# Optimization experiments

Hardware: AMD Instinct MI355X
Metric: run time of the kernel (lower is better)

Reference implementation:

```python
import jax, jax.numpy as jnp
import numpy as np

N_SIGMA = 1
K_MAX = 8          # max number of non-zero instance ids
FG_W = 1.0         # foreground_weight
W_INST, W_VAR, W_SEED = 1.0, 10.0, 1.0


def _lovasz_hinge_flat(logits, labels_f):
    # logits, labels_f: [P] flat; standard Lovasz hinge (descending-error sort)
    signs = 2.0 * labels_f - 1.0
    errors = 1.0 - logits * signs
    perm = jnp.argsort(-errors)
    errors_sorted = errors[perm]
    gt_sorted = labels_f[perm]
    gts = gt_sorted.sum()
    cum = jnp.cumsum(gt_sorted)
    intersection = gts - cum
    union = gts + jnp.cumsum(1.0 - gt_sorted)
    jaccard = 1.0 - intersection / union
    grad = jnp.concatenate([jaccard[:1], jaccard[1:] - jaccard[:-1]])
    return jnp.sum(jax.nn.relu(errors_sorted) * jax.lax.stop_gradient(grad))


def _spatial_emb_loss(prediction, instances, labels):
    B, C, H, W = prediction.shape
    inst = instances[:, 0]  # [B,H,W]
    # coordinate buffer: linspace over the full 1024x2048 grid, then sliced
    xm = jnp.linspace(0.0, 2.0, 2048)[:W]
    ym = jnp.linspace(0.0, 1.0, 1024)[:H]
    xym = jnp.stack([jnp.broadcast_to(xm[None, :], (H, W)),
                     jnp.broadcast_to(ym[:, None], (H, W))])  # [2,H,W]
    ids = jnp.arange(1, K_MAX + 1)

    def per_image(pred, ins, lab):
        spatial_emb = jnp.tanh(pred[0:2]) + xym            # [2,H,W]
        sigma = pred[2]                                     # [H,W] (n_sigma=1)
        seed = jax.nn.sigmoid(pred[3])                      # [H,W]
        bg = (lab == 0)
        seed_loss_bg = jnp.sum(jnp.where(bg, seed ** 2, 0.0))
        masks = (ins[None] == ids[:, None, None])           # [K,H,W]
        mf = masks.astype(pred.dtype)
        counts = mf.sum((1, 2))                             # [K]
        present = counts > 0
        cnt = jnp.maximum(counts, 1.0)
        # to_center=True: center = mean of xym over instance pixels
        center = jnp.einsum('chw,khw->kc', xym, mf) / cnt[:, None]   # [K,2]
        s_mean = jnp.einsum('hw,khw->k', sigma, mf) / cnt            # [K]
        var_k = jnp.einsum('khw,khw->k',
                           (sigma[None] - jax.lax.stop_gradient(s_mean)[:, None, None]) ** 2,
                           mf) / cnt
        s_exp = jnp.exp(10.0 * s_mean)                                # [K]
        d2 = jnp.sum((spatial_emb[None] - center[:, :, None, None]) ** 2, axis=1)  # [K,H,W]
        dist = jnp.exp(-s_exp[:, None, None] * d2)                    # [K,H,W]
        lov = jax.vmap(_lovasz_hinge_flat)(2.0 * dist.reshape(K_MAX, -1) - 1.0,
                                           mf.reshape(K_MAX, -1))     # [K]
        seed_fg = jnp.einsum('khw,khw->k',
                             (seed[None] - jax.lax.stop_gradient(dist)) ** 2, mf)
        objf = jnp.maximum(present.sum().astype(pred.dtype), 1.0)
        inst_loss = jnp.where(present, lov, 0.0).sum() / objf
        var_loss = jnp.where(present, var_k, 0.0).sum() / objf
        seed_loss = (seed_loss_bg + FG_W * jnp.where(present, seed_fg, 0.0).sum()) / (H * W)
        return W_INST * inst_loss + W_VAR * var_loss + W_SEED * seed_loss

    per = jax.vmap(per_image)(prediction, inst, labels)
    return per.mean() + 0.0 * prediction.sum()


def setup_inputs() -> dict:
    key = jax.random.key(0)
    k1, k2, k3 = jax.random.split(key, 3)
    B, H, W = 4, 512, 1024
    prediction = jax.random.normal(k1, (B, 2 + N_SIGMA + 1, H, W), dtype=jnp.float32)
    instances = jax.random.randint(k2, (B, 1, H, W), 0, K_MAX + 1, dtype=jnp.int32)
    labels = jax.random.randint(k3, (B, H, W), 0, 2, dtype=jnp.int32)
    return {"prediction": prediction, "instances": instances, "labels": labels}


def reference(prediction, instances, labels):
    return _spatial_emb_loss(prediction, instances, labels)
```

## Files before the change

### kernel.cpp

```cpp
#include <hip/hip_runtime.h>
#include <math.h>

namespace {
constexpr int B_ = 4, K_ = 8, H_ = 512, W_ = 1024;
constexpr int N_ = H_ * W_;
constexpr int M_ = 256;
constexpr int MP_ = M_ + 1;
constexpr int BK_ = B_ * K_;
constexpr int KM_ = K_ * M_;

constexpr int HB_ = 1024;
constexpr int HBPB_ = HB_ / B_;
constexpr int HCH_ = N_ / HBPB_;
constexpr int SB_ = 1024;
constexpr int SBPB_ = SB_ / B_;
constexpr int SCH_ = N_ / SBPB_;
constexpr int NSTAT = 41;

constexpr size_t PART_BYTES = (size_t)HB_ * KM_ * 4;
constexpr size_t SFG_OFF_B  = PART_BYTES;
constexpr size_t PSTAT_OFF_B = SFG_OFF_B + (size_t)BK_ * HBPB_ * 4;
constexpr size_t WSF_OFF_B  = PSTAT_OFF_B + (size_t)B_ * NSTAT * SBPB_ * 4;

constexpr int CNT_OFF  = 0;
constexpr int OBJF_OFF = 32;
}

__device__ __forceinline__ float fsigmoid_(float x) { return 1.0f / (1.0f + __expf(-x)); }
__device__ __forceinline__ float ftanh_(float x) { return 1.0f - 2.0f / (__expf(2.0f * x) + 1.0f); }

__global__ __launch_bounds__(256) void stats_kernel(const float* __restrict__ pred,
                                                    const int* __restrict__ inst,
                                                    const int* __restrict__ lab,
                                                    float* __restrict__ pstat,
                                                    float* __restrict__ out) {
    int tid = threadIdx.x;
    if (blockIdx.x == 0 && tid == 0) out[0] = 0.0f;
    int b = blockIdx.x >> 8;
    int blk = blockIdx.x & (SBPB_ - 1);
    int pix0 = blk * SCH_;

    const float* sigp = pred + ((long long)b * 4 + 2) * N_;
    const float* p3p  = pred + ((long long)b * 4 + 3) * N_;
    const int*   insp = inst + (long long)b * N_;
    const int*   labp = lab  + (long long)b * N_;

    float acc[NSTAT];
#pragma unroll
    for (int i = 0; i < NSTAT; i++) acc[i] = 0.0f;

#pragma unroll
    for (int it = 0; it < SCH_ / (256 * 4); it++) {
        int base = pix0 + (it * 256 + tid) * 4;
        float4 sg = *(const float4*)(sigp + base);
        float4 q3 = *(const float4*)(p3p + base);
        int4 in4 = *(const int4*)(insp + base);
        int4 lb4 = *(const int4*)(labp + base);
        float ss[4] = {sg.x, sg.y, sg.z, sg.w};
        float qq[4] = {q3.x, q3.y, q3.z, q3.w};
        int ii[4] = {in4.x, in4.y, in4.z, in4.w};
        int ll[4] = {lb4.x, lb4.y, lb4.z, lb4.w};
#pragma unroll
        for (int j = 0; j < 4; j++) {
            int pix = base + j;
            float xm = (float)(pix & (W_ - 1)) * (2.0f / 2047.0f);
            float ym = (float)(pix >> 10) * (1.0f / 1023.0f);
            float seed = fsigmoid_(qq[j]);
            if (ll[j] == 0) acc[40] += seed * seed;
            float s = ss[j];
#pragma unroll
            for (int k = 0; k < K_; k++) {
                float m = (ii[j] == k + 1) ? 1.0f : 0.0f;
                acc[k * 5]     += m;
                acc[k * 5 + 1] += m * xm;
                acc[k * 5 + 2] += m * ym;
                acc[k * 5 + 3] += m * s;
                acc[k * 5 + 4] += m * s * s;
            }
        }
    }
#pragma unroll
    for (int i = 0; i < NSTAT; i++) {
        float v = acc[i];
#pragma unroll
        for (int off = 32; off; off >>= 1) v += __shfl_down(v, off, 64);
        acc[i] = v;
    }
    __shared__ float xw[4][NSTAT];
    if ((tid & 63) == 0) {
        int w = tid >> 6;
#pragma unroll
        for (int i = 0; i < NSTAT; i++) xw[w][i] = acc[i];
    }
    __syncthreads();
    if (tid < NSTAT)
        pstat[((b * NSTAT + tid) << 8) + blk] =
            xw[0][tid] + xw[1][tid] + xw[2][tid] + xw[3][tid];
}

__global__ __launch_bounds__(256) void hist_kernel(const float* __restrict__ pred,
                                                   const int* __restrict__ inst,
                                                   const float* __restrict__ pstat,
                                                   float* __restrict__ wsf,
                                                   unsigned int* __restrict__ partial,
                                                   float* __restrict__ sfgpart,
                                                   float* __restrict__ out) {
    __shared__ float sq[NSTAT][4];
    __shared__ float ssum[NSTAT];
    __shared__ float prm[K_][4];
    __shared__ float svar[K_];
    __shared__ int spres[K_];
    __shared__ unsigned int hsh[K_ * MP_];
    __shared__ float xfg[4][K_];

    int tid = threadIdx.x;
    int b = blockIdx.x >> 8;
    int blk = blockIdx.x & (HBPB_ - 1);
    int pix0 = blk * HCH_;

    if (tid < NSTAT * 4) {
        int row = tid >> 2, q = tid & 3;
        const float4* p = (const float4*)(pstat + ((size_t)(b * NSTAT + row) << 8)) + q * 16;
        float4 a = {0, 0, 0, 0};
#pragma unroll
        for (int j = 0; j < 16; j++) {
            float4 v = p[j];
            a.x += v.x; a.y += v.y; a.z += v.z; a.w += v.w;
        }
        sq[row][q] = (a.x + a.y) + (a.z + a.w);
    }
    for (int i = tid; i < K_ * MP_; i += 256) hsh[i] = 0u;
    __syncthreads();
    if (tid < NSTAT) ssum[tid] = (sq[tid][0] + sq[tid][1]) + (sq[tid][2] + sq[tid][3]);
    __syncthreads();
    if (tid < K_) {
        float counts = ssum[tid * 5];
        float cnt = fmaxf(counts, 1.0f);
        float smean = ssum[tid * 5 + 3] / cnt;
        prm[tid][0] = ssum[tid * 5 + 1] / cnt;
        prm[tid][1] = ssum[tid * 5 + 2] / cnt;
        prm[tid][2] = expf(10.0f * smean);
        prm[tid][3] = counts;
        if (blk == 0) {
            svar[tid] = (counts > 0.0f) ? ssum[tid * 5 + 4] / cnt - smean * smean : 0.0f;
            spres[tid] = counts > 0.0f ? 1 : 0;
            wsf[CNT_OFF + b * K_ + tid] = counts;
        }
    }
    __syncthreads();
    if (blk == 0 && tid == 0) {
        float np = 0.0f, vl = 0.0f;
#pragma unroll
        for (int k = 0; k < K_; k++) { np += (float)spres[k]; vl += svar[k]; }
        float objf = fmaxf(np, 1.0f);
        wsf[OBJF_OFF + b] = objf;
        atomicAdd(out, (10.0f * vl / objf + ssum[40] / (float)N_) * (1.0f / (float)B_));
    }

    float cx[K_], cy[K_], sxp[K_];
    bool prs[K_];
#pragma unroll
    for (int k = 0; k < K_; k++) {
        cx[k] = prm[k][0]; cy[k] = prm[k][1]; sxp[k] = prm[k][2];
        prs[k] = prm[k][3] > 0.0f;
    }

    const float* p0p = pred + ((long long)b * 4) * N_;
    const float* p1p = p0p + N_;
    const float* p3p = p0p + 3LL * N_;
    const int* insp = inst + (long long)b * N_;

    float sfg[K_];
#pragma unroll
    for (int k = 0; k < K_; k++) sfg[k] = 0.0f;

#pragma unroll
    for (int it = 0; it < HCH_ / (256 * 4); it++) {
        int base = pix0 + (it * 256 + tid) * 4;
        float4 a0 = *(const float4*)(p0p + base);
        float4 a1 = *(const float4*)(p1p + base);
        float4 a3 = *(const float4*)(p3p + base);
        int4 in4 = *(const int4*)(insp + base);
        float v0[4] = {a0.x, a0.y, a0.z, a0.w};
        float v1[4] = {a1.x, a1.y, a1.z, a1.w};
        float v3[4] = {a3.x, a3.y, a3.z, a3.w};
        int ii[4] = {in4.x, in4.y, in4.z, in4.w};
#pragma unroll
        for (int j = 0; j < 4; j++) {
            int pix = base + j;
            float sex = ftanh_(v0[j]) + (float)(pix & (W_ - 1)) * (2.0f / 2047.0f);
            float sey = ftanh_(v1[j]) + (float)(pix >> 10) * (1.0f / 1023.0f);
            float seed = fsigmoid_(v3[j]);
            int ins = ii[j];
#pragma unroll
            for (int k = 0; k < K_; k++) {
                if (prs[k]) {
                    float dx = sex - cx[k];
                    float dy = sey - cy[k];
                    float dist = __expf(-sxp[k] * (dx * dx + dy * dy));
                    bool fg = (ins == k + 1);
                    int ib = (int)fminf(256.0f * dist, 255.0f);
                    int bin = fg ? 255 - ib : ib;
                    atomicAdd(&hsh[k * MP_ + bin], fg ? 0x10001u : 1u);
                    if (fg) { float d = seed - dist; sfg[k] += d * d; }
                }
            }
        }
    }
    __syncthreads();

    unsigned int* gp = partial + (size_t)blockIdx.x * KM_;
    for (int i = tid; i < KM_; i += 256)
        gp[i] = hsh[(i >> 8) * MP_ + (i & (M_ - 1))];

#pragma unroll
    for (int k = 0; k < K_; k++) {
        float v = sfg[k];
#pragma unroll
        for (int off = 32; off; off >>= 1) v += __shfl_down(v, off, 64);
        sfg[k] = v;
    }
    if ((tid & 63) == 0) {
        int w = tid >> 6;
#pragma unroll
        for (int k = 0; k < K_; k++) xfg[w][k] = sfg[k];
    }
    __syncthreads();
    if (tid < K_)
        sfgpart[(size_t)(b * K_ + tid) * HBPB_ + blk] =
            xfg[0][tid] + xfg[1][tid] + xfg[2][tid] + xfg[3][tid];
}

__global__ __launch_bounds__(1024) void lovasz_kernel(const unsigned int* __restrict__ partial,
                                                      const float* __restrict__ sfgpart,
                                                      const float* __restrict__ wsf,
                                                      float* __restrict__ out) {
    int bk = blockIdx.x;
    int b = bk >> 3, k = bk & 7;
    int tid = threadIdx.x;
    int bin = tid & 255, grp = tid >> 8;
    constexpr int PER = HBPB_ / 4;

    const unsigned int* p = partial +
        (size_t)(b * HBPB_ + grp * PER) * KM_ + k * M_ + bin;
    unsigned int n = 0, f = 0;
#pragma unroll 8
    for (int j = 0; j < PER; j++) {
        unsigned int v = p[(size_t)j * KM_];
        n += v & 0xffffu;
        f += v >> 16;
    }

    __shared__ unsigned int gn[4][256], gf[4][256];
    __shared__ unsigned int sn[256], sf[256];
    __shared__ float sacc[256];
    __shared__ float xs[4];
    gn[grp][bin] = n; gf[grp][bin] = f;
    __syncthreads();
    if (grp == 0) {
        sn[bin] = (gn[0][bin] + gn[1][bin]) + (gn[2][bin] + gn[3][bin]);
        sf[bin] = (gf[0][bin] + gf[1][bin]) + (gf[2][bin] + gf[3][bin]);
    }
    __syncthreads();

#pragma unroll
    for (int s = 1; s < 256; s <<= 1) {
        unsigned int an = 0, af = 0, bn = 0, bf = 0;
        if (tid < 256) {
            an = sn[tid]; af = sf[tid];
            if (tid + s < 256) { bn = sn[tid + s]; bf = sf[tid + s]; }
        }
        __syncthreads();
        if (tid < 256) { sn[tid] = an + bn; sf[tid] = af + bf; }
        __syncthreads();
    }

    float pcnt = wsf[CNT_OFF + bk];
    float pp = fmaxf(pcnt, 1.0f);
    if (tid < 256) {
        unsigned int R = sn[tid], F = sf[tid];
        float J = (R == 0) ? 0.0f : (1.0f - (pp - (float)F) / (pp + (float)(R - F)));
        sacc[tid] = (tid == 0 ? 0.5f : 1.0f) * J;
    }
    __syncthreads();
    for (int s = 128; s > 0; s >>= 1) {
        if (tid < s) sacc[tid] += sacc[tid + s];
        __syncthreads();
    }

    float sv = (tid < 256) ? sfgpart[(size_t)bk * HBPB_ + tid] : 0.0f;
#pragma unroll
    for (int off = 32; off; off >>= 1) sv += __shfl_down(sv, off, 64);
    if (tid < 256 && (tid & 63) == 0) xs[tid >> 6] = sv;
    __syncthreads();

    if (tid == 0 && pcnt > 0.0f) {
        float lov = sacc[0] * (2.0f / (float)M_);
        float sfgt = (xs[0] + xs[1]) + (xs[2] + xs[3]);
        float objf = wsf[OBJF_OFF + b];
        atomicAdd(out, (lov / objf + sfgt / (float)N_) * (1.0f / (float)B_));
    }
}

extern "C" void kernel_launch(void* const* d_in, const int* in_sizes, int n_in,
                              void* d_out, int out_size, void* d_ws, size_t ws_size,
                              hipStream_t stream) {
    const float* pred = (const float*)d_in[0];
    const int* inst = (const int*)d_in[1];
    const int* lab = (const int*)d_in[2];
    float* out = (float*)d_out;

    unsigned int* partial = (unsigned int*)d_ws;
    float* sfgpart = (float*)((char*)d_ws + SFG_OFF_B);
    float* pstat = (float*)((char*)d_ws + PSTAT_OFF_B);
    float* wsf = (float*)((char*)d_ws + WSF_OFF_B);

    stats_kernel<<<SB_, 256, 0, stream>>>(pred, inst, lab, pstat, out);
    hist_kernel<<<HB_, 256, 0, stream>>>(pred, inst, pstat, wsf, partial, sfgpart, out);
    lovasz_kernel<<<BK_, 1024, 0, stream>>>(partial, sfgpart, wsf, out);
}
```

Measured before the change: 121.1 us.

## Fuse three kernels into one cooperative kernel with grid syncs and split Lovasz reduction

Merges the stats, histogram and Lovasz kernels into a single cooperative launch separated by grid-wide syncs, removing two kernel launch boundaries. The stats phase swaps its 40 per-thread register accumulators for shared-memory float atomics on per-wave slots, touching only the instance a pixel belongs to. The histogram reduction is split into a sliced partial-sum phase spread across many blocks, followed by a small final scan, instead of 32 blocks each reading everything. The trade-offs are grid-sync cost, contention on the shared atomics, larger shared-memory use, and a grid that depends on the occupancy query; if fewer blocks fit, each runs several work units in a loop.

```diff
diff --git a/kernel.cpp b/kernel.cpp
--- a/kernel.cpp
+++ b/kernel.cpp
@@ -1,110 +1,45 @@
 #include <hip/hip_runtime.h>
+#include <hip/hip_cooperative_groups.h>
 #include <math.h>
 
+namespace cg = cooperative_groups;
+
 namespace {
-constexpr int B_ = 4, K_ = 8, H_ = 512, W_ = 1024;
-constexpr int N_ = H_ * W_;
+constexpr int B_ = 4, K_ = 8, W_ = 1024;
+constexpr int N_ = 512 * 1024;
 constexpr int M_ = 256;
 constexpr int MP_ = M_ + 1;
 constexpr int BK_ = B_ * K_;
 constexpr int KM_ = K_ * M_;
 
-constexpr int HB_ = 1024;
-constexpr int HBPB_ = HB_ / B_;
-constexpr int HCH_ = N_ / HBPB_;
-constexpr int SB_ = 1024;
-constexpr int SBPB_ = SB_ / B_;
-constexpr int SCH_ = N_ / SBPB_;
+constexpr int US_ = 1024, SBPB_ = 256, SCH_ = 2048;
+constexpr int UH_ = 1024, HBPB_ = 256, HCH_ = 2048;
 constexpr int NSTAT = 41;
-
-constexpr size_t PART_BYTES = (size_t)HB_ * KM_ * 4;
-constexpr size_t SFG_OFF_B  = PART_BYTES;
-constexpr size_t PSTAT_OFF_B = SFG_OFF_B + (size_t)BK_ * HBPB_ * 4;
-constexpr size_t WSF_OFF_B  = PSTAT_OFF_B + (size_t)B_ * NSTAT * SBPB_ * 4;
-
-constexpr int CNT_OFF  = 0;
-constexpr int OBJF_OFF = 32;
+constexpr int SLICES_ = 32, PERS_ = 8;
+
+constexpr size_t PART_SZ  = (size_t)UH_ * KM_ * 4;
+constexpr size_t SFG_B    = PART_SZ;
+constexpr size_t PSTAT_B  = SFG_B + (size_t)BK_ * HBPB_ * 4;
+constexpr size_t RED_B    = PSTAT_B + (size_t)B_ * NSTAT * SBPB_ * 4;
+constexpr size_t WSF_B    = RED_B + (size_t)BK_ * SLICES_ * M_ * 4;
+
+constexpr int CNT_OFF = 0, OBJF_OFF = 32;
 }
 
 __device__ __forceinline__ float fsigmoid_(float x) { return 1.0f / (1.0f + __expf(-x)); }
 __device__ __forceinline__ float ftanh_(float x) { return 1.0f - 2.0f / (__expf(2.0f * x) + 1.0f); }
 
-__global__ __launch_bounds__(256) void stats_kernel(const float* __restrict__ pred,
-                                                    const int* __restrict__ inst,
-                                                    const int* __restrict__ lab,
-                                                    float* __restrict__ pstat,
-                                                    float* __restrict__ out) {
+__global__ __launch_bounds__(256) void fused_kernel(
+    const float* __restrict__ pred, const int* __restrict__ inst,
+    const int* __restrict__ lab, float* __restrict__ pstat,
+    unsigned int* __restrict__ partial, float* __restrict__ sfgpart,
+    unsigned int* __restrict__ red, float* __restrict__ wsf,
+    float* __restrict__ out)
+{
+    cg::grid_group gg = cg::this_grid();
     int tid = threadIdx.x;
-    if (blockIdx.x == 0 && tid == 0) out[0] = 0.0f;
-    int b = blockIdx.x >> 8;
-    int blk = blockIdx.x & (SBPB_ - 1);
-    int pix0 = blk * SCH_;
-
-    const float* sigp = pred + ((long long)b * 4 + 2) * N_;
-    const float* p3p  = pred + ((long long)b * 4 + 3) * N_;
-    const int*   insp = inst + (long long)b * N_;
-    const int*   labp = lab  + (long long)b * N_;
-
-    float acc[NSTAT];
-#pragma unroll
-    for (int i = 0; i < NSTAT; i++) acc[i] = 0.0f;
-
-#pragma unroll
-    for (int it = 0; it < SCH_ / (256 * 4); it++) {
-        int base = pix0 + (it * 256 + tid) * 4;
-        float4 sg = *(const float4*)(sigp + base);
-        float4 q3 = *(const float4*)(p3p + base);
-        int4 in4 = *(const int4*)(insp + base);
-        int4 lb4 = *(const int4*)(labp + base);
-        float ss[4] = {sg.x, sg.y, sg.z, sg.w};
-        float qq[4] = {q3.x, q3.y, q3.z, q3.w};
-        int ii[4] = {in4.x, in4.y, in4.z, in4.w};
-        int ll[4] = {lb4.x, lb4.y, lb4.z, lb4.w};
-#pragma unroll
-        for (int j = 0; j < 4; j++) {
-            int pix = base + j;
-            float xm = (float)(pix & (W_ - 1)) * (2.0f / 2047.0f);
-            float ym = (float)(pix >> 10) * (1.0f / 1023.0f);
-            float seed = fsigmoid_(qq[j]);
-            if (ll[j] == 0) acc[40] += seed * seed;
-            float s = ss[j];
-#pragma unroll
-            for (int k = 0; k < K_; k++) {
-                float m = (ii[j] == k + 1) ? 1.0f : 0.0f;
-                acc[k * 5]     += m;
-                acc[k * 5 + 1] += m * xm;
-                acc[k * 5 + 2] += m * ym;
-                acc[k * 5 + 3] += m * s;
-                acc[k * 5 + 4] += m * s * s;
-            }
-        }
-    }
-#pragma unroll
-    for (int i = 0; i < NSTAT; i++) {
-        float v = acc[i];
-#pragma unroll
-        for (int off = 32; off; off >>= 1) v += __shfl_down(v, off, 64);
-        acc[i] = v;
-    }
-    __shared__ float xw[4][NSTAT];
-    if ((tid & 63) == 0) {
-        int w = tid >> 6;
-#pragma unroll
-        for (int i = 0; i < NSTAT; i++) xw[w][i] = acc[i];
-    }
-    __syncthreads();
-    if (tid < NSTAT)
-        pstat[((b * NSTAT + tid) << 8) + blk] =
-            xw[0][tid] + xw[1][tid] + xw[2][tid] + xw[3][tid];
-}
-
-__global__ __launch_bounds__(256) void hist_kernel(const float* __restrict__ pred,
-                                                   const int* __restrict__ inst,
-                                                   const float* __restrict__ pstat,
-                                                   float* __restrict__ wsf,
-                                                   unsigned int* __restrict__ partial,
-                                                   float* __restrict__ sfgpart,
-                                                   float* __restrict__ out) {
+
+    __shared__ float ws1[4 * 48];
     __shared__ float sq[NSTAT][4];
     __shared__ float ssum[NSTAT];
     __shared__ float prm[K_][4];
@@ -112,193 +47,240 @@
     __shared__ int spres[K_];
     __shared__ unsigned int hsh[K_ * MP_];
     __shared__ float xfg[4][K_];
-
-    int tid = threadIdx.x;
-    int b = blockIdx.x >> 8;
-    int blk = blockIdx.x & (HBPB_ - 1);
-    int pix0 = blk * HCH_;
-
-    if (tid < NSTAT * 4) {
-        int row = tid >> 2, q = tid & 3;
-        const float4* p = (const float4*)(pstat + ((size_t)(b * NSTAT + row) << 8)) + q * 16;
-        float4 a = {0, 0, 0, 0};
-#pragma unroll
-        for (int j = 0; j < 16; j++) {
-            float4 v = p[j];
-            a.x += v.x; a.y += v.y; a.z += v.z; a.w += v.w;
-        }
-        sq[row][q] = (a.x + a.y) + (a.z + a.w);
-    }
-    for (int i = tid; i < K_ * MP_; i += 256) hsh[i] = 0u;
-    __syncthreads();
-    if (tid < NSTAT) ssum[tid] = (sq[tid][0] + sq[tid][1]) + (sq[tid][2] + sq[tid][3]);
-    __syncthreads();
-    if (tid < K_) {
-        float counts = ssum[tid * 5];
-        float cnt = fmaxf(counts, 1.0f);
-        float smean = ssum[tid * 5 + 3] / cnt;
-        prm[tid][0] = ssum[tid * 5 + 1] / cnt;
-        prm[tid][1] = ssum[tid * 5 + 2] / cnt;
-        prm[tid][2] = expf(10.0f * smean);
-        prm[tid][3] = counts;
-        if (blk == 0) {
-            svar[tid] = (counts > 0.0f) ? ssum[tid * 5 + 4] / cnt - smean * smean : 0.0f;
-            spres[tid] = counts > 0.0f ? 1 : 0;
-            wsf[CNT_OFF + b * K_ + tid] = counts;
-        }
-    }
-    __syncthreads();
-    if (blk == 0 && tid == 0) {
-        float np = 0.0f, vl = 0.0f;
-#pragma unroll
-        for (int k = 0; k < K_; k++) { np += (float)spres[k]; vl += svar[k]; }
-        float objf = fmaxf(np, 1.0f);
-        wsf[OBJF_OFF + b] = objf;
-        atomicAdd(out, (10.0f * vl / objf + ssum[40] / (float)N_) * (1.0f / (float)B_));
-    }
-
-    float cx[K_], cy[K_], sxp[K_];
-    bool prs[K_];
-#pragma unroll
-    for (int k = 0; k < K_; k++) {
-        cx[k] = prm[k][0]; cy[k] = prm[k][1]; sxp[k] = prm[k][2];
-        prs[k] = prm[k][3] > 0.0f;
-    }
-
-    const float* p0p = pred + ((long long)b * 4) * N_;
-    const float* p1p = p0p + N_;
-    const float* p3p = p0p + 3LL * N_;
-    const int* insp = inst + (long long)b * N_;
-
-    float sfg[K_];
-#pragma unroll
-    for (int k = 0; k < K_; k++) sfg[k] = 0.0f;
-
-#pragma unroll
-    for (int it = 0; it < HCH_ / (256 * 4); it++) {
-        int base = pix0 + (it * 256 + tid) * 4;
-        float4 a0 = *(const float4*)(p0p + base);
-        float4 a1 = *(const float4*)(p1p + base);
-        float4 a3 = *(const float4*)(p3p + base);
-        int4 in4 = *(const int4*)(insp + base);
-        float v0[4] = {a0.x, a0.y, a0.z, a0.w};
-        float v1[4] = {a1.x, a1.y, a1.z, a1.w};
-        float v3[4] = {a3.x, a3.y, a3.z, a3.w};
-        int ii[4] = {in4.x, in4.y, in4.z, in4.w};
-#pragma unroll
-        for (int j = 0; j < 4; j++) {
-            int pix = base + j;
-            float sex = ftanh_(v0[j]) + (float)(pix & (W_ - 1)) * (2.0f / 2047.0f);
-            float sey = ftanh_(v1[j]) + (float)(pix >> 10) * (1.0f / 1023.0f);
-            float seed = fsigmoid_(v3[j]);
-            int ins = ii[j];
-#pragma unroll
-            for (int k = 0; k < K_; k++) {
-                if (prs[k]) {
-                    float dx = sex - cx[k];
-                    float dy = sey - cy[k];
-                    float dist = __expf(-sxp[k] * (dx * dx + dy * dy));
-                    bool fg = (ins == k + 1);
-                    int ib = (int)fminf(256.0f * dist, 255.0f);
-                    int bin = fg ? 255 - ib : ib;
-                    atomicAdd(&hsh[k * MP_ + bin], fg ? 0x10001u : 1u);
-                    if (fg) { float d = seed - dist; sfg[k] += d * d; }
-                }
-            }
-        }
-    }
-    __syncthreads();
-
-    unsigned int* gp = partial + (size_t)blockIdx.x * KM_;
-    for (int i = tid; i < KM_; i += 256)
-        gp[i] = hsh[(i >> 8) * MP_ + (i & (M_ - 1))];
-
-#pragma unroll
-    for (int k = 0; k < K_; k++) {
-        float v = sfg[k];
-#pragma unroll
-        for (int off = 32; off; off >>= 1) v += __shfl_down(v, off, 64);
-        sfg[k] = v;
-    }
-    if ((tid & 63) == 0) {
-        int w = tid >> 6;
-#pragma unroll
-        for (int k = 0; k < K_; k++) xfg[w][k] = sfg[k];
-    }
-    __syncthreads();
-    if (tid < K_)
-        sfgpart[(size_t)(b * K_ + tid) * HBPB_ + blk] =
-            xfg[0][tid] + xfg[1][tid] + xfg[2][tid] + xfg[3][tid];
-}
-
-__global__ __launch_bounds__(1024) void lovasz_kernel(const unsigned int* __restrict__ partial,
-                                                      const float* __restrict__ sfgpart,
-                                                      const float* __restrict__ wsf,
-                                                      float* __restrict__ out) {
-    int bk = blockIdx.x;
-    int b = bk >> 3, k = bk & 7;
-    int tid = threadIdx.x;
-    int bin = tid & 255, grp = tid >> 8;
-    constexpr int PER = HBPB_ / 4;
-
-    const unsigned int* p = partial +
-        (size_t)(b * HBPB_ + grp * PER) * KM_ + k * M_ + bin;
-    unsigned int n = 0, f = 0;
-#pragma unroll 8
-    for (int j = 0; j < PER; j++) {
-        unsigned int v = p[(size_t)j * KM_];
-        n += v & 0xffffu;
-        f += v >> 16;
-    }
-
-    __shared__ unsigned int gn[4][256], gf[4][256];
     __shared__ unsigned int sn[256], sf[256];
     __shared__ float sacc[256];
     __shared__ float xs[4];
-    gn[grp][bin] = n; gf[grp][bin] = f;
-    __syncthreads();
-    if (grp == 0) {
-        sn[bin] = (gn[0][bin] + gn[1][bin]) + (gn[2][bin] + gn[3][bin]);
-        sf[bin] = (gf[0][bin] + gf[1][bin]) + (gf[2][bin] + gf[3][bin]);
+
+    for (unsigned int u = blockIdx.x; u < US_; u += gridDim.x) {
+        if (u == 0 && tid == 0) out[0] = 0.0f;
+        int b = u >> 8, blk = u & (SBPB_ - 1);
+        int pix0 = blk * SCH_;
+        if (tid < 192) ws1[tid] = 0.0f;
+        __syncthreads();
+        float* wacc = ws1 + (tid >> 6) * 48;
+
+        const float* sigp = pred + ((long long)b * 4 + 2) * N_;
+        const float* p3p  = pred + ((long long)b * 4 + 3) * N_;
+        const int*   insp = inst + (long long)b * N_;
+        const int*   labp = lab  + (long long)b * N_;
+
+        float bg = 0.0f;
+#pragma unroll
+        for (int it = 0; it < SCH_ / (256 * 4); it++) {
+            int base = pix0 + (it * 256 + tid) * 4;
+            float4 sg = *(const float4*)(sigp + base);
+            float4 q3 = *(const float4*)(p3p + base);
+            int4 in4 = *(const int4*)(insp + base);
+            int4 lb4 = *(const int4*)(labp + base);
+            float ss[4] = {sg.x, sg.y, sg.z, sg.w};
+            float qq[4] = {q3.x, q3.y, q3.z, q3.w};
+            int ii[4] = {in4.x, in4.y, in4.z, in4.w};
+            int ll[4] = {lb4.x, lb4.y, lb4.z, lb4.w};
+#pragma unroll
+            for (int j = 0; j < 4; j++) {
+                float seed = fsigmoid_(qq[j]);
+                if (ll[j] == 0) bg += seed * seed;
+                int ins = ii[j];
+                if (ins > 0) {
+                    int pix = base + j;
+                    float xm = (float)(pix & (W_ - 1)) * (2.0f / 2047.0f);
+                    float ym = (float)(pix >> 10) * (1.0f / 1023.0f);
+                    float s = ss[j];
+                    int s0 = (ins - 1) * 5;
+                    atomicAdd(&wacc[s0], 1.0f);
+                    atomicAdd(&wacc[s0 + 1], xm);
+                    atomicAdd(&wacc[s0 + 2], ym);
+                    atomicAdd(&wacc[s0 + 3], s);
+                    atomicAdd(&wacc[s0 + 4], s * s);
+                }
+            }
+        }
+#pragma unroll
+        for (int off = 32; off; off >>= 1) bg += __shfl_down(bg, off, 64);
+        if ((tid & 63) == 0) wacc[40] = bg;
+        __syncthreads();
+        if (tid < NSTAT)
+            pstat[((b * NSTAT + tid) << 8) + blk] =
+                ws1[tid] + ws1[48 + tid] + ws1[96 + tid] + ws1[144 + tid];
+        __syncthreads();
     }
-    __syncthreads();
-
-#pragma unroll
-    for (int s = 1; s < 256; s <<= 1) {
-        unsigned int an = 0, af = 0, bn = 0, bf = 0;
-        if (tid < 256) {
-            an = sn[tid]; af = sf[tid];
+    gg.sync();
+
+    for (unsigned int u = blockIdx.x; u < UH_; u += gridDim.x) {
+        int b = u >> 8, blk = u & (HBPB_ - 1);
+        int pix0 = blk * HCH_;
+
+        if (tid < NSTAT * 4) {
+            int row = tid >> 2, q = tid & 3;
+            const float4* p = (const float4*)(pstat + ((size_t)(b * NSTAT + row) << 8)) + q * 16;
+            float4 a = {0, 0, 0, 0};
+#pragma unroll
+            for (int j = 0; j < 16; j++) {
+                float4 v = p[j];
+                a.x += v.x; a.y += v.y; a.z += v.z; a.w += v.w;
+            }
+            sq[row][q] = (a.x + a.y) + (a.z + a.w);
+        }
+        for (int i = tid; i < K_ * MP_; i += 256) hsh[i] = 0u;
+        __syncthreads();
+        if (tid < NSTAT) ssum[tid] = (sq[tid][0] + sq[tid][1]) + (sq[tid][2] + sq[tid][3]);
+        __syncthreads();
+        if (tid < K_) {
+            float counts = ssum[tid * 5];
+            float cnt = fmaxf(counts, 1.0f);
+            float smean = ssum[tid * 5 + 3] / cnt;
+            prm[tid][0] = ssum[tid * 5 + 1] / cnt;
+            prm[tid][1] = ssum[tid * 5 + 2] / cnt;
+            prm[tid][2] = expf(10.0f * smean);
+            prm[tid][3] = counts;
+            if (blk == 0) {
+                svar[tid] = (counts > 0.0f) ? ssum[tid * 5 + 4] / cnt - smean * smean : 0.0f;
+                spres[tid] = counts > 0.0f ? 1 : 0;
+                wsf[CNT_OFF + b * K_ + tid] = counts;
+            }
+        }
+        __syncthreads();
+        if (blk == 0 && tid == 0) {
+            float np = 0.0f, vl = 0.0f;
+#pragma unroll
+            for (int k = 0; k < K_; k++) { np += (float)spres[k]; vl += svar[k]; }
+            float objf = fmaxf(np, 1.0f);
+            wsf[OBJF_OFF + b] = objf;
+            atomicAdd(out, (10.0f * vl / objf + ssum[40] / (float)N_) * (1.0f / (float)B_));
+        }
+
+        float cx[K_], cy[K_], sxp[K_];
+        bool prs[K_];
+#pragma unroll
+        for (int k = 0; k < K_; k++) {
+            cx[k] = prm[k][0]; cy[k] = prm[k][1]; sxp[k] = prm[k][2];
+            prs[k] = prm[k][3] > 0.0f;
+        }
+
+        const float* p0p = pred + ((long long)b * 4) * N_;
+        const float* p1p = p0p + N_;
+        const float* p3p = p0p + 3LL * N_;
+        const int* insp = inst + (long long)b * N_;
+
+        float sfg[K_];
+#pragma unroll
+        for (int k = 0; k < K_; k++) sfg[k] = 0.0f;
+
+#pragma unroll
+        for (int it = 0; it < HCH_ / (256 * 4); it++) {
+            int base = pix0 + (it * 256 + tid) * 4;
+            float4 a0 = *(const float4*)(p0p + base);
+            float4 a1 = *(const float4*)(p1p + base);
+            float4 a3 = *(const float4*)(p3p + base);
+            int4 in4 = *(const int4*)(insp + base);
+            float v0[4] = {a0.x, a0.y, a0.z, a0.w};
+            float v1[4] = {a1.x, a1.y, a1.z, a1.w};
+            float v3[4] = {a3.x, a3.y, a3.z, a3.w};
+            int ii[4] = {in4.x, in4.y, in4.z, in4.w};
+#pragma unroll
+            for (int j = 0; j < 4; j++) {
+                int pix = base + j;
+                float sex = ftanh_(v0[j]) + (float)(pix & (W_ - 1)) * (2.0f / 2047.0f);
+                float sey = ftanh_(v1[j]) + (float)(pix >> 10) * (1.0f / 1023.0f);
+                float seed = fsigmoid_(v3[j]);
+                int ins = ii[j];
+#pragma unroll
+                for (int k = 0; k < K_; k++) {
+                    if (prs[k]) {
+                        float dx = sex - cx[k];
+                        float dy = sey - cy[k];
+                        float dist = __expf(-sxp[k] * (dx * dx + dy * dy));
+                        bool fg = (ins == k + 1);
+                        int ib = (int)fminf(256.0f * dist, 255.0f);
+                        int bin = fg ? 255 - ib : ib;
+                        atomicAdd(&hsh[k * MP_ + bin], fg ? 0x10001u : 1u);
+                        if (fg) { float d = seed - dist; sfg[k] += d * d; }
+                    }
+                }
+            }
+        }
+        __syncthreads();
+
+        unsigned int* gp = partial + (size_t)u * KM_;
+        for (int i = tid; i < KM_; i += 256)
+            gp[i] = hsh[(i >> 8) * MP_ + (i & (M_ - 1))];
+
+#pragma unroll
+        for (int k = 0; k < K_; k++) {
+            float v = sfg[k];
+#pragma unroll
+            for (int off = 32; off; off >>= 1) v += __shfl_down(v, off, 64);
+            sfg[k] = v;
+        }
+        if ((tid & 63) == 0) {
+            int w = tid >> 6;
+#pragma unroll
+            for (int k = 0; k < K_; k++) xfg[w][k] = sfg[k];
+        }
+        __syncthreads();
+        if (tid < K_)
+            sfgpart[(size_t)(b * K_ + tid) * HBPB_ + blk] =
+                xfg[0][tid] + xfg[1][tid] + xfg[2][tid] + xfg[3][tid];
+        __syncthreads();
+    }
+    gg.sync();
+
+    for (unsigned int u = blockIdx.x; u < BK_ * SLICES_; u += gridDim.x) {
+        int bk = u >> 5, s = u & (SLICES_ - 1);
+        int b = bk >> 3, k = bk & 7;
+        const unsigned int* p = partial + (size_t)(b * HBPB_ + s * PERS_) * KM_ + k * M_ + tid;
+        unsigned int n = 0, f = 0;
+#pragma unroll
+        for (int j = 0; j < PERS_; j++) {
+            unsigned int v = p[(size_t)j * KM_];
+            n += v & 0xffffu;
+            f += v >> 16;
+        }
+        red[(size_t)u * M_ + tid] = (f << 16) | n;
+    }
+    gg.sync();
+
+    for (unsigned int u = blockIdx.x; u < BK_; u += gridDim.x) {
+        int bk = u, b = bk >> 3;
+        const unsigned int* rp = red + (size_t)bk * SLICES_ * M_ + tid;
+        unsigned int n = 0, f = 0;
+#pragma unroll
+        for (int s = 0; s < SLICES_; s++) {
+            unsigned int v = rp[s * M_];
+            n += v & 0xffffu;
+            f += v >> 16;
+        }
+        sn[tid] = n; sf[tid] = f;
+        __syncthreads();
+#pragma unroll
+        for (int s = 1; s < 256; s <<= 1) {
+            unsigned int an = sn[tid], af = sf[tid], bn = 0, bf = 0;
             if (tid + s < 256) { bn = sn[tid + s]; bf = sf[tid + s]; }
-        }
-        __syncthreads();
-        if (tid < 256) { sn[tid] = an + bn; sf[tid] = af + bf; }
-        __syncthreads();
-    }
-
-    float pcnt = wsf[CNT_OFF + bk];
-    float pp = fmaxf(pcnt, 1.0f);
-    if (tid < 256) {
+            __syncthreads();
+            sn[tid] = an + bn; sf[tid] = af + bf;
+            __syncthreads();
+        }
+        float pcnt = wsf[CNT_OFF + bk];
+        float pp = fmaxf(pcnt, 1.0f);
         unsigned int R = sn[tid], F = sf[tid];
         float J = (R == 0) ? 0.0f : (1.0f - (pp - (float)F) / (pp + (float)(R - F)));
         sacc[tid] = (tid == 0 ? 0.5f : 1.0f) * J;
-    }
-    __syncthreads();
-    for (int s = 128; s > 0; s >>= 1) {
-        if (tid < s) sacc[tid] += sacc[tid + s];
-        __syncthreads();
-    }
-
-    float sv = (tid < 256) ? sfgpart[(size_t)bk * HBPB_ + tid] : 0.0f;
-#pragma unroll
-    for (int off = 32; off; off >>= 1) sv += __shfl_down(sv, off, 64);
-    if (tid < 256 && (tid & 63) == 0) xs[tid >> 6] = sv;
-    __syncthreads();
-
-    if (tid == 0 && pcnt > 0.0f) {
-        float lov = sacc[0] * (2.0f / (float)M_);
-        float sfgt = (xs[0] + xs[1]) + (xs[2] + xs[3]);
-        float objf = wsf[OBJF_OFF + b];
-        atomicAdd(out, (lov / objf + sfgt / (float)N_) * (1.0f / (float)B_));
+        __syncthreads();
+        for (int s = 128; s > 0; s >>= 1) {
+            if (tid < s) sacc[tid] += sacc[tid + s];
+            __syncthreads();
+        }
+        float sv = sfgpart[(size_t)bk * HBPB_ + tid];
+#pragma unroll
+        for (int off = 32; off; off >>= 1) sv += __shfl_down(sv, off, 64);
+        if ((tid & 63) == 0) xs[tid >> 6] = sv;
+        __syncthreads();
+        if (tid == 0 && pcnt > 0.0f) {
+            float lov = sacc[0] * (2.0f / (float)M_);
+            float sfgt = (xs[0] + xs[1]) + (xs[2] + xs[3]);
+            atomicAdd(out, (lov / wsf[OBJF_OFF + b] + sfgt / (float)N_) * (1.0f / (float)B_));
+        }
+        __syncthreads();
     }
 }
 
@@ -311,11 +293,18 @@
     float* out = (float*)d_out;
 
     unsigned int* partial = (unsigned int*)d_ws;
-    float* sfgpart = (float*)((char*)d_ws + SFG_OFF_B);
-    float* pstat = (float*)((char*)d_ws + PSTAT_OFF_B);
-    float* wsf = (float*)((char*)d_ws + WSF_OFF_B);
-
-    stats_kernel<<<SB_, 256, 0, stream>>>(pred, inst, lab, pstat, out);
-    hist_kernel<<<HB_, 256, 0, stream>>>(pred, inst, pstat, wsf, partial, sfgpart, out);
-    lovasz_kernel<<<BK_, 1024, 0, stream>>>(partial, sfgpart, wsf, out);
+    float* sfgpart = (float*)((char*)d_ws + SFG_B);
+    float* pstat = (float*)((char*)d_ws + PSTAT_B);
+    unsigned int* red = (unsigned int*)((char*)d_ws + RED_B);
+    float* wsf = (float*)((char*)d_ws + WSF_B);
+
+    int nb = 0;
+    hipOccupancyMaxActiveBlocksPerMultiprocessor(&nb, fused_kernel, 256, 0);
+    if (nb < 1) nb = 1;
+    unsigned int grid = (unsigned int)nb * 256u;
+    if (grid > 1024u) grid = 1024u;
+
+    void* args[] = {&pred, &inst, &lab, &pstat, &partial, &sfgpart, &red, &wsf, &out};
+    hipLaunchCooperativeKernel((const void*)fused_kernel, dim3(grid), dim3(256),
+                               args, 0, stream);
 }
```

After: 316.3 us. +161.3%, slower.
